# Kernel optimization log

Hardware: AMD Instinct MI355X
Metric: run time of the kernel (lower is better)

Reference implementation:

```python
import jax, jax.numpy as jnp
import numpy as np

N = 200_000      # nodes
E = 6_400_000    # edges (avg degree 32)
ATT = 16         # scorer hidden dim
MAXD = 512       # mixer max_depth
C = 1.0          # curvature
EPS = 1e-15


def _mobius_add(a, b, c):
    # Mobius addition on the Poincare ball: a (+)_c b
    ab = jnp.sum(a * b, axis=-1, keepdims=True)
    aa = jnp.sum(a * a, axis=-1, keepdims=True)
    bb = jnp.sum(b * b, axis=-1, keepdims=True)
    num = (1.0 + 2.0 * c * ab + c * bb) * a + (1.0 - c * aa) * b
    den = 1.0 + 2.0 * c * ab + (c * c) * aa * bb
    return num / jnp.maximum(den, EPS)


def setup_inputs() -> dict:
    key = jax.random.key(0)
    ks = jax.random.split(key, 8)
    x = jax.random.normal(ks[0], (N, 2), dtype=jnp.float32)
    # keep nodes strictly inside the unit Poincare disk (|x| < 0.5)
    x = 0.5 * x / (1.0 + jnp.linalg.norm(x, axis=-1, keepdims=True))
    edge_index = jax.random.randint(ks[1], (2, E), 0, N, dtype=jnp.int32)
    depth = jax.random.randint(ks[2], (N,), 0, MAXD, dtype=jnp.int32)
    W1 = jax.random.normal(ks[3], (2, ATT), dtype=jnp.float32) * (1.0 / np.sqrt(2.0))
    b1 = jnp.zeros((ATT,), dtype=jnp.float32)
    W2 = jax.random.normal(ks[4], (ATT, 1), dtype=jnp.float32) * (1.0 / np.sqrt(ATT))
    eta = jnp.array(1.0, dtype=jnp.float32)
    depth_scale = 1.0 + 0.1 * jax.random.normal(ks[5], (MAXD, 1), dtype=jnp.float32)
    depth_theta = 0.1 * jax.random.normal(ks[6], (MAXD, 1), dtype=jnp.float32)
    return dict(x=x, edge_index=edge_index, depth=depth, W1=W1, b1=b1, W2=W2,
                eta=eta, depth_scale=depth_scale, depth_theta=depth_theta)


def reference(x, edge_index, depth, W1, b1, W2, eta, depth_scale, depth_theta):
    c = C
    sc = jnp.sqrt(jnp.asarray(c, dtype=x.dtype))
    row, col = edge_index[0], edge_index[1]
    xi = x[row]   # [E,2] target node of each edge
    xj = x[col]   # [E,2] source node of each edge

    # log_{xi}(xj): tangent vector at xi
    u = _mobius_add(-xi, xj, c)                                        # [E,2]
    un = jnp.maximum(jnp.linalg.norm(u, axis=-1, keepdims=True), EPS)  # [E,1]
    lam_i = 2.0 / jnp.maximum(1.0 - c * jnp.sum(xi * xi, axis=-1, keepdims=True), EPS)
    v = (2.0 / (sc * lam_i)) * jnp.arctanh(jnp.minimum(sc * un, 1.0 - 1e-5)) * (u / un)

    # tiny MLP attention score per edge
    h = jax.nn.gelu(v @ W1 + b1, approximate=False)   # [E,ATT]
    scores = (h @ W2)[:, 0]                           # [E]

    # segment softmax over edges grouped by target node `row`
    smax = jax.ops.segment_max(scores, row, num_segments=N)
    ex = jnp.exp(scores - smax[row])
    denom = jax.ops.segment_sum(ex, row, num_segments=N)
    alpha = ex / jnp.maximum(denom[row], 1e-15)       # [E]

    # weighted scatter-add of tangent vectors
    m = jax.ops.segment_sum(alpha[:, None] * v, row, num_segments=N)   # [N,2]

    # depth-gated rotation/scale in the tangent space (mixer)
    d = jnp.clip(depth, 0, MAXD - 1)
    k = depth_scale[d]            # [N,1]
    ang = depth_theta[d][:, 0]    # [N]
    ca, sa = jnp.cos(ang), jnp.sin(ang)
    m = k * jnp.stack([ca * m[:, 0] - sa * m[:, 1],
                       sa * m[:, 0] + ca * m[:, 1]], axis=-1)

    # exp_{x}(eta * m)
    w = eta * m
    wn = jnp.maximum(jnp.linalg.norm(w, axis=-1, keepdims=True), EPS)
    lam_x = 2.0 / jnp.maximum(1.0 - c * jnp.sum(x * x, axis=-1, keepdims=True), EPS)
    second = jnp.tanh(sc * lam_x * wn / 2.0) * (w / (sc * wn))
    return _mobius_add(x, second, c)
```

## Files before the change

kernel.cpp:

```cpp
#include <hip/hip_runtime.h>
#include <hip/hip_fp16.h>
#include <math.h>

#define EPSF 1e-15f
#define BSH  8
#define BSZ  (1 << BSH)
#define BMSK (BSZ - 1)
#define CAPB 9216
#define MAXNB 1024
#define AGG_T 1024
#define BIN_T 1024
#define LCH   6400

#define TBL   128
#define TW    129
#define VMIN  (-1.2f)
#define VH    (2.4f / 128.0f)
#define INVH  (128.0f / 2.4f)

__device__ __forceinline__ float fast_rcp(float x)  { return __builtin_amdgcn_rcpf(x); }
__device__ __forceinline__ float fast_rsq(float x)  { return __builtin_amdgcn_rsqf(x); }
__device__ __forceinline__ float fast_exp(float x)  { return __builtin_amdgcn_exp2f(x * 1.4426950408889634f); }

__device__ __forceinline__ unsigned int float_to_ordered(float f) {
    unsigned int u = __float_as_uint(f);
    return (u & 0x80000000u) ? ~u : (u | 0x80000000u);
}
__device__ __forceinline__ float ordered_to_float(unsigned int u) {
    u = (u & 0x80000000u) ? (u & 0x7FFFFFFFu) : ~u;
    return __uint_as_float(u);
}

__device__ __forceinline__ void edge_v_fast(float2 xi, float2 xj, float& vx, float& vy) {
    float ab = -(xi.x * xj.x + xi.y * xj.y);
    float aa = xi.x * xi.x + xi.y * xi.y;
    float bb = xj.x * xj.x + xj.y * xj.y;
    float f1 = 1.0f + 2.0f * ab + bb;
    float f2 = 1.0f - aa;
    float ux = f1 * (-xi.x) + f2 * xj.x;
    float uy = f1 * (-xi.y) + f2 * xj.y;
    float den = 1.0f + 2.0f * ab + aa * bb;
    float inv_den = fast_rcp(fmaxf(den, EPSF));
    ux *= inv_den; uy *= inv_den;
    float un2 = fmaxf(ux * ux + uy * uy, 1e-24f);
    float inv_un = fast_rsq(un2);
    float un = fminf(un2 * inv_un, 1.0f - 1e-5f);
    float t = 0.34657359027997264f * __builtin_amdgcn_logf((1.0f + un) * fast_rcp(1.0f - un));
    float s = fmaxf(f2, EPSF) * t * inv_un;
    vx = s * ux; vy = s * uy;
}

__device__ __forceinline__ void edge_v(float2 xi, float2 xj, float& vx, float& vy) {
    float ab = -(xi.x * xj.x + xi.y * xj.y);
    float aa = xi.x * xi.x + xi.y * xi.y;
    float bb = xj.x * xj.x + xj.y * xj.y;
    float f1 = 1.0f + 2.0f * ab + bb;
    float f2 = 1.0f - aa;
    float ux = f1 * (-xi.x) + f2 * xj.x;
    float uy = f1 * (-xi.y) + f2 * xj.y;
    float den = 1.0f + 2.0f * ab + aa * bb;
    float inv_den = 1.0f / fmaxf(den, EPSF);
    ux *= inv_den; uy *= inv_den;
    float un = fmaxf(sqrtf(ux * ux + uy * uy), EPSF);
    float t  = atanhf(fminf(un, 1.0f - 1e-5f));
    float s = fmaxf(f2, EPSF) * t / un;
    vx = s * ux; vy = s * uy;
}

__device__ __forceinline__ float edge_score(float vx, float vy,
                                            const float* __restrict__ W1,
                                            const float* __restrict__ b1,
                                            const float* __restrict__ W2) {
    float score = 0.0f;
#pragma unroll
    for (int k = 0; k < 16; ++k) {
        float z = fmaf(vx, W1[k], fmaf(vy, W1[16 + k], b1[k]));
        float g = 0.5f * z * (1.0f + erff(z * 0.70710678118654752f));
        score = fmaf(g, W2[k], score);
    }
    return score;
}

__device__ __forceinline__ float2 finalize_node(float2 xv, float mx, float my,
                                                int d, float eta,
                                                const float* __restrict__ dscale,
                                                const float* __restrict__ dtheta) {
    d = d < 0 ? 0 : (d > 511 ? 511 : d);
    float k   = dscale[d];
    float ang = dtheta[d];
    float ca = cosf(ang), sa = sinf(ang);
    float m0 = k * (ca * mx - sa * my);
    float m1 = k * (sa * mx + ca * my);

    float wx = eta * m0, wy = eta * m1;
    float wn = fmaxf(sqrtf(wx * wx + wy * wy), 1e-15f);

    float aa = xv.x * xv.x + xv.y * xv.y;
    float lam = 2.0f / fmaxf(1.0f - aa, 1e-15f);
    float fac = tanhf(lam * wn * 0.5f) / wn;
    float sx = fac * wx, sy = fac * wy;

    float ab = xv.x * sx + xv.y * sy;
    float bb = sx * sx + sy * sy;
    float n1 = 1.0f + 2.0f * ab + bb;
    float n2 = 1.0f - aa;
    float ox = n1 * xv.x + n2 * sx;
    float oy = n1 * xv.y + n2 * sy;
    float dd = 1.0f + 2.0f * ab + aa * bb;
    float inv = 1.0f / fmaxf(dd, 1e-15f);
    return make_float2(ox * inv, oy * inv);
}


__global__ void init_cursor(unsigned* __restrict__ cursor, int NB) {
    int b = blockIdx.x * blockDim.x + threadIdx.x;
    if (b < NB) cursor[b] = (unsigned)b * CAPB;
}

__global__ void build_score_table(const float* __restrict__ W1,
                                  const float* __restrict__ b1,
                                  const float* __restrict__ W2,
                                  float* __restrict__ tbl) {
    int i = blockIdx.x * blockDim.x + threadIdx.x;
    if (i >= TW * TW) return;
    int iy = i / TW, ix = i - iy * TW;
    float vx = VMIN + VH * (float)ix;
    float vy = VMIN + VH * (float)iy;
    tbl[i] = edge_score(vx, vy, W1, b1, W2);
}

__global__ __launch_bounds__(BIN_T)
void bin_edges(const int* __restrict__ ei,
               unsigned* __restrict__ cursor,
               unsigned* __restrict__ sorted,
               int E, int NB) {
    __shared__ unsigned bkrank[LCH];
    __shared__ unsigned payload[LCH];
    __shared__ unsigned sortedLoc[LCH];
    __shared__ unsigned gdst[LCH];
    __shared__ unsigned hist[MAXNB];
    __shared__ unsigned scanA[MAXNB];
    __shared__ unsigned loc[MAXNB];
    __shared__ unsigned gbase[MAXNB];

    int tid = threadIdx.x;
    int e0 = blockIdx.x * LCH;
    int cnt = min(E - e0, LCH);
    if (cnt <= 0) return;

    if (tid < MAXNB) hist[tid] = 0;
    __syncthreads();

    for (int idx = tid; idx < cnt; idx += BIN_T) {
        int r = ei[e0 + idx];
        int c = ei[E + e0 + idx];
        unsigned bk = (unsigned)r >> BSH;
        unsigned rank = atomicAdd(&hist[bk], 1u);
        bkrank[idx] = (bk << 14) | rank;
        payload[idx] = ((unsigned)(r & BMSK) << 24) | (unsigned)c;
    }
    __syncthreads();

    unsigned h = (tid < MAXNB) ? hist[tid] : 0u;
    if (tid < MAXNB) scanA[tid] = h;
    __syncthreads();
#pragma unroll
    for (int step = 1; step < MAXNB; step <<= 1) {
        unsigned v = 0u;
        if (tid < MAXNB) {
            v = scanA[tid];
            if (tid >= step) v += scanA[tid - step];
        }
        __syncthreads();
        if (tid < MAXNB) scanA[tid] = v;
        __syncthreads();
    }
    if (tid < MAXNB) {
        loc[tid] = scanA[tid] - h;
        gbase[tid] = h ? atomicAdd(&cursor[tid], h) : 0u;
    }
    __syncthreads();

    for (int idx = tid; idx < cnt; idx += BIN_T) {
        unsigned v = bkrank[idx];
        unsigned bk = v >> 14;
        unsigned rank = v & 0x3FFFu;
        unsigned pos = loc[bk] + rank;
        sortedLoc[pos] = payload[idx];
        unsigned g = gbase[bk] + rank;
        gdst[pos] = (g < (bk + 1u) * CAPB) ? g : 0xFFFFFFFFu;
    }
    __syncthreads();

    for (int idx = tid; idx < cnt; idx += BIN_T) {
        unsigned g = gdst[idx];
        if (g != 0xFFFFFFFFu) sorted[g] = sortedLoc[idx];
    }
}

__global__ __launch_bounds__(AGG_T, 8)
void aggregate(const float2* __restrict__ x,
               const unsigned* __restrict__ cursor,
               const unsigned* __restrict__ sorted,
               const int* __restrict__ depth,
               const float* __restrict__ tbl,
               const float* __restrict__ etaPtr,
               const float* __restrict__ dscale,
               const float* __restrict__ dtheta,
               float2* __restrict__ out, int N) {
    __shared__ float2 xr[BSZ];
    __shared__ unsigned stashA[CAPB];
    __shared__ unsigned stashV[CAPB];
    __shared__ unsigned nmax[BSZ];
    __shared__ unsigned long long accP[BSZ];

    int b = blockIdx.x;
    int tid = threadIdx.x;
    int nb0 = b << BSH;
    int nodeCnt = min(BSZ, N - nb0);
    if (tid < BSZ) {
        nmax[tid] = 0u;
        accP[tid] = 0ull;
        if (tid < nodeCnt) xr[tid] = x[nb0 + tid];
    }
    __syncthreads();

    unsigned basep = (unsigned)b * CAPB;
    unsigned cnt = cursor[b] - basep;
    cnt = cnt > (unsigned)CAPB ? (unsigned)CAPB : cnt;

    for (unsigned i = tid; i < cnt; i += AGG_T) {
        unsigned u = sorted[basep + i];
        int rl = (int)(u >> 24);
        int c  = (int)(u & 0xFFFFFFu);
        float2 xi = xr[rl];
        float2 xj = x[c];
        float vx, vy;
        edge_v_fast(xi, xj, vx, vy);

        float tx = fminf(fmaxf((vx - VMIN) * INVH, 0.0f), 127.999f);
        float ty = fminf(fmaxf((vy - VMIN) * INVH, 0.0f), 127.999f);
        int ix = (int)tx, iy = (int)ty;
        float fx = tx - (float)ix, fy = ty - (float)iy;
        const float* row = tbl + iy * TW + ix;
        float s00 = row[0], s01 = row[1];
        float s10 = row[TW], s11 = row[TW + 1];
        float sA = fmaf(fx, s01 - s00, s00);
        float sB = fmaf(fx, s11 - s10, s10);
        float score = fmaf(fy, sB - sA, sA);

        __half hs = __float2half_rn(score);
        float sq = __half2float(hs);
        unsigned short s16 = *(unsigned short*)&hs;
        __half2 h2 = __floats2half2_rn(vx, vy);
        stashA[i] = ((unsigned)rl << 16) | (unsigned)s16;
        stashV[i] = *(unsigned*)&h2;
        atomicMax(&nmax[rl], float_to_ordered(sq));
    }
    __syncthreads();

    for (unsigned i = tid; i < cnt; i += AGG_T) {
        unsigned a = stashA[i];
        int rl = (int)(a >> 16);
        unsigned short s16 = (unsigned short)(a & 0xFFFFu);
        __half hs = *(__half*)&s16;
        float s = __half2float(hs);
        float mxs = ordered_to_float(nmax[rl]);
        float ex = fast_exp(s - mxs);
        unsigned vv = stashV[i];
        __half2 h2 = *(__half2*)&vv;
        float2 v2 = __half22float2(h2);
        unsigned e0 = __float2uint_rn(ex * 16384.0f);
        unsigned e1 = __float2uint_rn(ex * (v2.x + 2.0f) * 0.25f * 16384.0f);
        unsigned e2 = __float2uint_rn(ex * (v2.y + 2.0f) * 0.25f * 16384.0f);
        unsigned long long pk = (unsigned long long)e0
                              | ((unsigned long long)e1 << 21)
                              | ((unsigned long long)e2 << 42);
        atomicAdd(&accP[rl], pk);
    }
    __syncthreads();

    if (tid >= nodeCnt) return;
    unsigned long long w = accP[tid];
    float F0 = (float)(unsigned int)(w & 0x1FFFFFull);
    float F1 = (float)(unsigned int)((w >> 21) & 0x1FFFFFull);
    float F2 = (float)(unsigned int)(w >> 42);
    float mx = 0.0f, my = 0.0f;
    if (F0 > 0.0f) {
        float inv = 1.0f / F0;
        mx = 4.0f * F1 * inv - 2.0f;
        my = 4.0f * F2 * inv - 2.0f;
    }
    int i = nb0 + tid;
    out[i] = finalize_node(xr[tid], mx, my, depth[i], etaPtr[0], dscale, dtheta);
}


__global__ void init_kernel(unsigned int* __restrict__ smax,
                            unsigned long long* __restrict__ maccP, int N) {
    int i = blockIdx.x * blockDim.x + threadIdx.x;
    if (i < N) {
        smax[i] = float_to_ordered(-INFINITY);
        maccP[i] = 0ull;
    }
}

__global__ void pass1_score_max(const float2* __restrict__ x,
                                const int* __restrict__ ei,
                                const float* __restrict__ W1,
                                const float* __restrict__ b1,
                                const float* __restrict__ W2,
                                unsigned int* __restrict__ smax, int E) {
    int e = blockIdx.x * blockDim.x + threadIdx.x;
    if (e >= E) return;
    int r = ei[e];
    int c = ei[E + e];
    float vx, vy;
    edge_v(x[r], x[c], vx, vy);
    float score = edge_score(vx, vy, W1, b1, W2);
    atomicMax(&smax[r], float_to_ordered(score));
}

#define PK_SCALE 16384.0f

__global__ void pass2_accum(const float2* __restrict__ x,
                            const int* __restrict__ ei,
                            const float* __restrict__ W1,
                            const float* __restrict__ b1,
                            const float* __restrict__ W2,
                            const unsigned int* __restrict__ smax,
                            unsigned long long* __restrict__ maccP, int E) {
    int e = blockIdx.x * blockDim.x + threadIdx.x;
    if (e >= E) return;
    int r = ei[e];
    int c = ei[E + e];
    float vx, vy;
    edge_v(x[r], x[c], vx, vy);
    float score = edge_score(vx, vy, W1, b1, W2);
    float mx = ordered_to_float(smax[r]);
    float ex = expf(score - mx);
    unsigned e0 = __float2uint_rn(ex * PK_SCALE);
    unsigned e1 = __float2uint_rn(ex * (vx + 2.0f) * 0.25f * PK_SCALE);
    unsigned e2 = __float2uint_rn(ex * (vy + 2.0f) * 0.25f * PK_SCALE);
    unsigned long long pk = (unsigned long long)e0
                          | ((unsigned long long)e1 << 21)
                          | ((unsigned long long)e2 << 42);
    atomicAdd(&maccP[r], pk);
}

__global__ void pass3_finalize(const float2* __restrict__ x,
                               const int* __restrict__ depth,
                               const unsigned long long* __restrict__ maccP,
                               const float* __restrict__ etaPtr,
                               const float* __restrict__ dscale,
                               const float* __restrict__ dtheta,
                               float2* __restrict__ out, int N) {
    int i = blockIdx.x * blockDim.x + threadIdx.x;
    if (i >= N) return;
    unsigned long long w = maccP[i];
    float F0 = (float)(unsigned int)(w & 0x1FFFFFull);
    float F1 = (float)(unsigned int)((w >> 21) & 0x1FFFFFull);
    float F2 = (float)(unsigned int)(w >> 42);
    float mx = 0.0f, my = 0.0f;
    if (F0 > 0.0f) {
        float inv = 1.0f / F0;
        mx = 4.0f * F1 * inv - 2.0f;
        my = 4.0f * F2 * inv - 2.0f;
    }
    out[i] = finalize_node(x[i], mx, my, depth[i], etaPtr[0], dscale, dtheta);
}


extern "C" void kernel_launch(void* const* d_in, const int* in_sizes, int n_in,
                              void* d_out, int out_size, void* d_ws, size_t ws_size,
                              hipStream_t stream) {
    const float2* x   = (const float2*)d_in[0];
    const int* ei     = (const int*)d_in[1];
    const int* depth  = (const int*)d_in[2];
    const float* W1   = (const float*)d_in[3];
    const float* b1   = (const float*)d_in[4];
    const float* W2   = (const float*)d_in[5];
    const float* eta  = (const float*)d_in[6];
    const float* dsc  = (const float*)d_in[7];
    const float* dth  = (const float*)d_in[8];
    float2* out = (float2*)d_out;

    int N = in_sizes[0] / 2;
    int E = in_sizes[1] / 2;
    int NB = (N + BSZ - 1) >> BSH;

    const int B = 256;
    size_t sortedBytes = (size_t)NB * CAPB * 4;
    size_t need = 4096 + sortedBytes + (size_t)TW * TW * 4;
    if (NB <= MAXNB && ws_size >= need) {
        unsigned* cursor = (unsigned*)d_ws;
        unsigned* sorted = (unsigned*)((char*)d_ws + 4096);
        float* tbl = (float*)((char*)d_ws + 4096 + sortedBytes);
        int binG = (E + LCH - 1) / LCH;
        init_cursor<<<(NB + B - 1) / B, B, 0, stream>>>(cursor, NB);
        build_score_table<<<(TW * TW + B - 1) / B, B, 0, stream>>>(W1, b1, W2, tbl);
        bin_edges<<<binG, BIN_T, 0, stream>>>(ei, cursor, sorted, E, NB);
        aggregate<<<NB, AGG_T, 0, stream>>>(x, cursor, sorted, depth, tbl,
                                            eta, dsc, dth, out, N);
    } else {
        unsigned long long* maccP = (unsigned long long*)d_ws;
        unsigned int* smax = (unsigned int*)(maccP + N);
        init_kernel<<<(N + B - 1) / B, B, 0, stream>>>(smax, maccP, N);
        pass1_score_max<<<(E + B - 1) / B, B, 0, stream>>>(x, ei, W1, b1, W2, smax, E);
        pass2_accum<<<(E + B - 1) / B, B, 0, stream>>>(x, ei, W1, b1, W2, smax, maccP, E);
        pass3_finalize<<<(N + B - 1) / B, B, 0, stream>>>(x, depth, maccP, eta, dsc, dth, out, N);
    }
}
```

Measured before the change: 195.3 us.

## Fuse table build into binning, vectorize edge loads, halve bin chunk size

Builds the score table inside the binning kernel instead of a separate launch. The per-bucket cursor now starts at zero via a memset rather than a kernel, so offsets are relative. Edge indices are loaded as int4 and the aggregate loop handles two edges per thread with uint2 loads and stores. The binning chunk is halved and launch bounds are raised, which adds more blocks and more global cursor atomics in exchange for higher occupancy.

```diff
diff --git a/kernel.cpp b/kernel.cpp
--- a/kernel.cpp
+++ b/kernel.cpp
@@ -10,7 +10,7 @@
 #define MAXNB 1024
 #define AGG_T 1024
 #define BIN_T 1024
-#define LCH   6400
+#define LCH   3200
 
 #define TBL   128
 #define TW    129
@@ -112,11 +112,6 @@
 }
 
 
-__global__ void init_cursor(unsigned* __restrict__ cursor, int NB) {
-    int b = blockIdx.x * blockDim.x + threadIdx.x;
-    if (b < NB) cursor[b] = (unsigned)b * CAPB;
-}
-
 __global__ void build_score_table(const float* __restrict__ W1,
                                   const float* __restrict__ b1,
                                   const float* __restrict__ W2,
@@ -129,13 +124,17 @@
     tbl[i] = edge_score(vx, vy, W1, b1, W2);
 }
 
-__global__ __launch_bounds__(BIN_T)
+__global__ __launch_bounds__(BIN_T, 8)
 void bin_edges(const int* __restrict__ ei,
                unsigned* __restrict__ cursor,
                unsigned* __restrict__ sorted,
-               int E, int NB) {
-    __shared__ unsigned bkrank[LCH];
-    __shared__ unsigned payload[LCH];
+               int E, int NB, int buildTbl,
+               const float* __restrict__ W1,
+               const float* __restrict__ b1,
+               const float* __restrict__ W2,
+               float* __restrict__ tbl) {
+    __shared__ __align__(16) unsigned bkrank[LCH];
+    __shared__ __align__(16) unsigned payload[LCH];
     __shared__ unsigned sortedLoc[LCH];
     __shared__ unsigned gdst[LCH];
     __shared__ unsigned hist[MAXNB];
@@ -144,6 +143,17 @@
     __shared__ unsigned gbase[MAXNB];
 
     int tid = threadIdx.x;
+
+    if (buildTbl) {
+        int gi = blockIdx.x * BIN_T + tid;
+        if (gi < TW * TW) {
+            int iy = gi / TW, ix = gi - iy * TW;
+            float vx = VMIN + VH * (float)ix;
+            float vy = VMIN + VH * (float)iy;
+            tbl[gi] = edge_score(vx, vy, W1, b1, W2);
+        }
+    }
+
     int e0 = blockIdx.x * LCH;
     int cnt = min(E - e0, LCH);
     if (cnt <= 0) return;
@@ -151,13 +161,48 @@
     if (tid < MAXNB) hist[tid] = 0;
     __syncthreads();
 
-    for (int idx = tid; idx < cnt; idx += BIN_T) {
-        int r = ei[e0 + idx];
-        int c = ei[E + e0 + idx];
-        unsigned bk = (unsigned)r >> BSH;
-        unsigned rank = atomicAdd(&hist[bk], 1u);
-        bkrank[idx] = (bk << 14) | rank;
-        payload[idx] = ((unsigned)(r & BMSK) << 24) | (unsigned)c;
+    if (((E | cnt) & 3) == 0) {
+        for (int idx = tid * 4; idx < cnt; idx += BIN_T * 4) {
+            const int4 r4 = *(const int4*)(ei + e0 + idx);
+            const int4 c4 = *(const int4*)(ei + E + e0 + idx);
+            unsigned br0, br1, br2, br3;
+            {
+                unsigned bk = (unsigned)r4.x >> BSH;
+                unsigned rank = atomicAdd(&hist[bk], 1u);
+                br0 = (bk << 14) | rank;
+            }
+            {
+                unsigned bk = (unsigned)r4.y >> BSH;
+                unsigned rank = atomicAdd(&hist[bk], 1u);
+                br1 = (bk << 14) | rank;
+            }
+            {
+                unsigned bk = (unsigned)r4.z >> BSH;
+                unsigned rank = atomicAdd(&hist[bk], 1u);
+                br2 = (bk << 14) | rank;
+            }
+            {
+                unsigned bk = (unsigned)r4.w >> BSH;
+                unsigned rank = atomicAdd(&hist[bk], 1u);
+                br3 = (bk << 14) | rank;
+            }
+            *(uint4*)(bkrank + idx) = make_uint4(br0, br1, br2, br3);
+            uint4 pl;
+            pl.x = ((unsigned)(r4.x & BMSK) << 24) | (unsigned)c4.x;
+            pl.y = ((unsigned)(r4.y & BMSK) << 24) | (unsigned)c4.y;
+            pl.z = ((unsigned)(r4.z & BMSK) << 24) | (unsigned)c4.z;
+            pl.w = ((unsigned)(r4.w & BMSK) << 24) | (unsigned)c4.w;
+            *(uint4*)(payload + idx) = pl;
+        }
+    } else {
+        for (int idx = tid; idx < cnt; idx += BIN_T) {
+            int r = ei[e0 + idx];
+            int c = ei[E + e0 + idx];
+            unsigned bk = (unsigned)r >> BSH;
+            unsigned rank = atomicAdd(&hist[bk], 1u);
+            bkrank[idx] = (bk << 14) | rank;
+            payload[idx] = ((unsigned)(r & BMSK) << 24) | (unsigned)c;
+        }
     }
     __syncthreads();
 
@@ -187,8 +232,8 @@
         unsigned rank = v & 0x3FFFu;
         unsigned pos = loc[bk] + rank;
         sortedLoc[pos] = payload[idx];
-        unsigned g = gbase[bk] + rank;
-        gdst[pos] = (g < (bk + 1u) * CAPB) ? g : 0xFFFFFFFFu;
+        unsigned rel = gbase[bk] + rank;
+        gdst[pos] = (rel < (unsigned)CAPB) ? (bk * (unsigned)CAPB + rel) : 0xFFFFFFFFu;
     }
     __syncthreads();
 
@@ -209,8 +254,8 @@
                const float* __restrict__ dtheta,
                float2* __restrict__ out, int N) {
     __shared__ float2 xr[BSZ];
-    __shared__ unsigned stashA[CAPB];
-    __shared__ unsigned stashV[CAPB];
+    __shared__ __align__(8) unsigned stashA[CAPB];
+    __shared__ __align__(8) unsigned stashV[CAPB];
     __shared__ unsigned nmax[BSZ];
     __shared__ unsigned long long accP[BSZ];
 
@@ -225,58 +270,108 @@
     }
     __syncthreads();
 
-    unsigned basep = (unsigned)b * CAPB;
-    unsigned cnt = cursor[b] - basep;
-    cnt = cnt > (unsigned)CAPB ? (unsigned)CAPB : cnt;
-
-    for (unsigned i = tid; i < cnt; i += AGG_T) {
-        unsigned u = sorted[basep + i];
-        int rl = (int)(u >> 24);
-        int c  = (int)(u & 0xFFFFFFu);
-        float2 xi = xr[rl];
-        float2 xj = x[c];
-        float vx, vy;
-        edge_v_fast(xi, xj, vx, vy);
-
-        float tx = fminf(fmaxf((vx - VMIN) * INVH, 0.0f), 127.999f);
-        float ty = fminf(fmaxf((vy - VMIN) * INVH, 0.0f), 127.999f);
-        int ix = (int)tx, iy = (int)ty;
-        float fx = tx - (float)ix, fy = ty - (float)iy;
-        const float* row = tbl + iy * TW + ix;
-        float s00 = row[0], s01 = row[1];
-        float s10 = row[TW], s11 = row[TW + 1];
-        float sA = fmaf(fx, s01 - s00, s00);
-        float sB = fmaf(fx, s11 - s10, s10);
-        float score = fmaf(fy, sB - sA, sA);
-
-        __half hs = __float2half_rn(score);
-        float sq = __half2float(hs);
-        unsigned short s16 = *(unsigned short*)&hs;
-        __half2 h2 = __floats2half2_rn(vx, vy);
-        stashA[i] = ((unsigned)rl << 16) | (unsigned)s16;
-        stashV[i] = *(unsigned*)&h2;
-        atomicMax(&nmax[rl], float_to_ordered(sq));
-    }
-    __syncthreads();
-
-    for (unsigned i = tid; i < cnt; i += AGG_T) {
-        unsigned a = stashA[i];
-        int rl = (int)(a >> 16);
-        unsigned short s16 = (unsigned short)(a & 0xFFFFu);
-        __half hs = *(__half*)&s16;
-        float s = __half2float(hs);
-        float mxs = ordered_to_float(nmax[rl]);
-        float ex = fast_exp(s - mxs);
-        unsigned vv = stashV[i];
-        __half2 h2 = *(__half2*)&vv;
-        float2 v2 = __half22float2(h2);
-        unsigned e0 = __float2uint_rn(ex * 16384.0f);
-        unsigned e1 = __float2uint_rn(ex * (v2.x + 2.0f) * 0.25f * 16384.0f);
-        unsigned e2 = __float2uint_rn(ex * (v2.y + 2.0f) * 0.25f * 16384.0f);
-        unsigned long long pk = (unsigned long long)e0
-                              | ((unsigned long long)e1 << 21)
-                              | ((unsigned long long)e2 << 42);
-        atomicAdd(&accP[rl], pk);
+    unsigned cnt = cursor[b];
+    if (cnt > (unsigned)CAPB) cnt = (unsigned)CAPB;
+    unsigned basep = (unsigned)b * (unsigned)CAPB;
+
+    for (unsigned i = (unsigned)tid * 2u; i < cnt; i += (unsigned)AGG_T * 2u) {
+        uint2 u2 = *(const uint2*)(sorted + basep + i);
+        bool has2 = (i + 1u) < cnt;
+
+        int rlA = (int)(u2.x >> 24);
+        int cA  = (int)(u2.x & 0xFFFFFFu);
+        int rlB = (int)(u2.y >> 24);
+        int cB  = has2 ? (int)(u2.y & 0xFFFFFFu) : cA;
+
+        float2 xiA = xr[rlA];
+        float2 xiB = xr[rlB];
+        float2 xjA = x[cA];
+        float2 xjB = x[cB];
+
+        float vxA, vyA, vxB, vyB;
+        edge_v_fast(xiA, xjA, vxA, vyA);
+        edge_v_fast(xiB, xjB, vxB, vyB);
+
+        float txA = fminf(fmaxf((vxA - VMIN) * INVH, 0.0f), 127.999f);
+        float tyA = fminf(fmaxf((vyA - VMIN) * INVH, 0.0f), 127.999f);
+        float txB = fminf(fmaxf((vxB - VMIN) * INVH, 0.0f), 127.999f);
+        float tyB = fminf(fmaxf((vyB - VMIN) * INVH, 0.0f), 127.999f);
+        int ixA = (int)txA, iyA = (int)tyA;
+        int ixB = (int)txB, iyB = (int)tyB;
+        float fxA = txA - (float)ixA, fyA = tyA - (float)iyA;
+        float fxB = txB - (float)ixB, fyB = tyB - (float)iyB;
+        const float* rowA = tbl + iyA * TW + ixA;
+        const float* rowB = tbl + iyB * TW + ixB;
+        float a00 = rowA[0], a01 = rowA[1], a10 = rowA[TW], a11 = rowA[TW + 1];
+        float b00 = rowB[0], b01 = rowB[1], b10 = rowB[TW], b11 = rowB[TW + 1];
+        float sAa = fmaf(fxA, a01 - a00, a00);
+        float sAb = fmaf(fxA, a11 - a10, a10);
+        float scoreA = fmaf(fyA, sAb - sAa, sAa);
+        float sBa = fmaf(fxB, b01 - b00, b00);
+        float sBb = fmaf(fxB, b11 - b10, b10);
+        float scoreB = fmaf(fyB, sBb - sBa, sBa);
+
+        __half hsA = __float2half_rn(scoreA);
+        __half hsB = __float2half_rn(scoreB);
+        unsigned short s16A = *(unsigned short*)&hsA;
+        unsigned short s16B = *(unsigned short*)&hsB;
+        __half2 h2A = __floats2half2_rn(vxA, vyA);
+        __half2 h2B = __floats2half2_rn(vxB, vyB);
+        unsigned pA = ((unsigned)rlA << 16) | (unsigned)s16A;
+        unsigned pB = ((unsigned)rlB << 16) | (unsigned)s16B;
+
+        if (has2) {
+            *(uint2*)(stashA + i) = make_uint2(pA, pB);
+            *(uint2*)(stashV + i) = make_uint2(*(unsigned*)&h2A, *(unsigned*)&h2B);
+            atomicMax(&nmax[rlA], float_to_ordered(__half2float(hsA)));
+            atomicMax(&nmax[rlB], float_to_ordered(__half2float(hsB)));
+        } else {
+            stashA[i] = pA;
+            stashV[i] = *(unsigned*)&h2A;
+            atomicMax(&nmax[rlA], float_to_ordered(__half2float(hsA)));
+        }
+    }
+    __syncthreads();
+
+    for (unsigned i = (unsigned)tid * 2u; i < cnt; i += (unsigned)AGG_T * 2u) {
+        uint2 a2 = *(const uint2*)(stashA + i);
+        uint2 v2 = *(const uint2*)(stashV + i);
+        bool has2 = (i + 1u) < cnt;
+
+        int rlA = (int)(a2.x >> 16);
+        int rlB = (int)((a2.y >> 16) & 0xFFu);
+        unsigned short s16A = (unsigned short)(a2.x & 0xFFFFu);
+        unsigned short s16B = (unsigned short)(a2.y & 0xFFFFu);
+        __half hsA = *(__half*)&s16A;
+        __half hsB = *(__half*)&s16B;
+        float sA = __half2float(hsA);
+        float sB = __half2float(hsB);
+        float mA = ordered_to_float(nmax[rlA]);
+        float mB = ordered_to_float(nmax[rlB]);
+        float exA = fast_exp(sA - mA);
+        float exB = fast_exp(sB - mB);
+        __half2 hvA = *(__half2*)&v2.x;
+        __half2 hvB = *(__half2*)&v2.y;
+        float2 vA = __half22float2(hvA);
+        float2 vB = __half22float2(hvB);
+
+        unsigned a0 = __float2uint_rn(exA * 16384.0f);
+        unsigned a1 = __float2uint_rn(exA * (vA.x + 2.0f) * 0.25f * 16384.0f);
+        unsigned a2i = __float2uint_rn(exA * (vA.y + 2.0f) * 0.25f * 16384.0f);
+        unsigned long long pkA = (unsigned long long)a0
+                               | ((unsigned long long)a1 << 21)
+                               | ((unsigned long long)a2i << 42);
+        atomicAdd(&accP[rlA], pkA);
+
+        if (has2) {
+            unsigned b0 = __float2uint_rn(exB * 16384.0f);
+            unsigned b1c = __float2uint_rn(exB * (vB.x + 2.0f) * 0.25f * 16384.0f);
+            unsigned b2c = __float2uint_rn(exB * (vB.y + 2.0f) * 0.25f * 16384.0f);
+            unsigned long long pkB = (unsigned long long)b0
+                                   | ((unsigned long long)b1c << 21)
+                                   | ((unsigned long long)b2c << 42);
+            atomicAdd(&accP[rlB], pkB);
+        }
     }
     __syncthreads();
 
@@ -397,9 +492,13 @@
         unsigned* sorted = (unsigned*)((char*)d_ws + 4096);
         float* tbl = (float*)((char*)d_ws + 4096 + sortedBytes);
         int binG = (E + LCH - 1) / LCH;
-        init_cursor<<<(NB + B - 1) / B, B, 0, stream>>>(cursor, NB);
-        build_score_table<<<(TW * TW + B - 1) / B, B, 0, stream>>>(W1, b1, W2, tbl);
-        bin_edges<<<binG, BIN_T, 0, stream>>>(ei, cursor, sorted, E, NB);
+        int tblBlocks = (TW * TW + BIN_T - 1) / BIN_T;
+        int buildInBin = (binG >= tblBlocks) ? 1 : 0;
+        hipMemsetAsync(cursor, 0, (size_t)NB * sizeof(unsigned), stream);
+        if (!buildInBin)
+            build_score_table<<<(TW * TW + B - 1) / B, B, 0, stream>>>(W1, b1, W2, tbl);
+        bin_edges<<<binG, BIN_T, 0, stream>>>(ei, cursor, sorted, E, NB, buildInBin,
+                                              W1, b1, W2, tbl);
         aggregate<<<NB, AGG_T, 0, stream>>>(x, cursor, sorted, depth, tbl,
                                             eta, dsc, dth, out, N);
     } else {
```

Result: slower. 204.8 us (+4.9%).
